# Kernel tuning notes

Measured on AMD Instinct MI355X. Metric: run time of the kernel, lower is better.

## Reference

```python
import jax, jax.numpy as jnp
import numpy as np

N, E, L, HEADS, HID = 50000, 600000, 4, 8, 128
IN_C, OUT_C = 64, 64
D_HEAD = HID // HEADS


def _layer_norm(x, g, b, eps=1e-5):
    m = jnp.mean(x, axis=-1, keepdims=True)
    v = jnp.mean((x - m) ** 2, axis=-1, keepdims=True)
    return (x - m) * jax.lax.rsqrt(v + eps) * g + b


def _transformer_conv(h, src, dst, Wq, bq, Wk, bk, Wv, bv, Ws, bs, Wbeta):
    # PyG TransformerConv with beta=True, concat=True. src=edge_index[0] (j), dst=edge_index[1] (i).
    n, f = h.shape
    q = (h @ Wq.T + bq)[dst].reshape(-1, HEADS, D_HEAD)   # [E,H,D] query at destination
    k = (h @ Wk.T + bk)[src].reshape(-1, HEADS, D_HEAD)   # [E,H,D] key at source
    v = (h @ Wv.T + bv)[src].reshape(-1, HEADS, D_HEAD)   # [E,H,D] value at source
    alpha = jnp.sum(q * k, axis=-1) / float(np.sqrt(D_HEAD))  # [E,H]
    amax = jax.ops.segment_max(alpha, dst, num_segments=n)     # [N,H] segment softmax (stable)
    ex = jnp.exp(alpha - amax[dst])
    denom = jax.ops.segment_sum(ex, dst, num_segments=n)
    a = ex / (denom[dst] + 1e-16)                              # [E,H]
    out = jax.ops.segment_sum((a[:, :, None] * v).reshape(-1, f), dst, num_segments=n)  # [N,F]
    x_r = h @ Ws.T + bs                                        # root/skip transform
    beta = jax.nn.sigmoid(jnp.concatenate([out, x_r, out - x_r], axis=-1) @ Wbeta.T)    # [N,1]
    return beta * x_r + (1.0 - beta) * out


def _forward(x, src, dst, Wi, bi, Wq, bq, Wk, bk, Wv, bv, Ws, bs, Wbeta, ln_g, ln_b, W1, b1, W2, b2, Wo, bo):
    h = jax.nn.gelu(x @ Wi.T + bi, approximate=False)
    for i in range(L):
        res = h
        h = _transformer_conv(h, src, dst, Wq[i], bq[i], Wk[i], bk[i], Wv[i], bv[i], Ws[i], bs[i], Wbeta[i])
        h = _layer_norm(h + res, ln_g[i], ln_b[i])
        res = h
        f = jax.nn.gelu(h @ W1[i].T + b1[i], approximate=False) @ W2[i].T + b2[i]
        h = f + res
    return h @ Wo.T + bo


def setup_inputs() -> dict:
    key = jax.random.key(0)
    ks = jax.random.split(key, 24)
    rn = lambda k, shp, s=0.05: (jax.random.normal(k, shp, jnp.float32) * s)
    x = jax.random.normal(ks[0], (N, IN_C), jnp.float32)
    edge_index = jax.random.randint(ks[1], (2, E), 0, N, dtype=jnp.int64)
    return {
        "x": x,
        "edge_index": edge_index,
        "Wi": rn(ks[2], (HID, IN_C)), "bi": jnp.zeros((HID,), jnp.float32),
        "Wq": rn(ks[3], (L, HID, HID)), "bq": jnp.zeros((L, HID), jnp.float32),
        "Wk": rn(ks[4], (L, HID, HID)), "bk": jnp.zeros((L, HID), jnp.float32),
        "Wv": rn(ks[5], (L, HID, HID)), "bv": jnp.zeros((L, HID), jnp.float32),
        "Ws": rn(ks[6], (L, HID, HID)), "bs": jnp.zeros((L, HID), jnp.float32),
        "Wbeta": rn(ks[7], (L, 1, 3 * HID)),
        "ln_g": jnp.ones((L, HID), jnp.float32), "ln_b": jnp.zeros((L, HID), jnp.float32),
        "W1": rn(ks[8], (L, 4 * HID, HID)), "b1": jnp.zeros((L, 4 * HID), jnp.float32),
        "W2": rn(ks[9], (L, HID, 4 * HID)), "b2": jnp.zeros((L, HID), jnp.float32),
        "Wo": rn(ks[10], (OUT_C, HID)), "bo": jnp.zeros((OUT_C,), jnp.float32),
    }


def reference(x, edge_index, Wi, bi, Wq, bq, Wk, bk, Wv, bv, Ws, bs, Wbeta, ln_g, ln_b, W1, b1, W2, b2, Wo, bo):
    src, dst = edge_index[0], edge_index[1]
    return _forward(x, src, dst, Wi, bi, Wq, bq, Wk, bk, Wv, bv, Ws, bs, Wbeta, ln_g, ln_b, W1, b1, W2, b2, Wo, bo)
```

## Files before the change

### kernel.cpp

```cpp
#include <hip/hip_runtime.h>
#include <cmath>

#define HIDC   128
#define LAYERS 4
#define IN_C   64
#define OUT_C  64

typedef _Float16 h16x8 __attribute__((ext_vector_type(8)));
typedef float    f32x4 __attribute__((ext_vector_type(4)));

__device__ __forceinline__ float gelu_f(float x) {
    return 0.5f * x * (1.0f + erff(x * 0.70710678118654752f));
}

__device__ __forceinline__ void cvt8(const float4& a, const float4& b, h16x8& h) {
    h[0]=(_Float16)a.x; h[1]=(_Float16)a.y; h[2]=(_Float16)a.z; h[3]=(_Float16)a.w;
    h[4]=(_Float16)b.x; h[5]=(_Float16)b.y; h[6]=(_Float16)b.z; h[7]=(_Float16)b.w;
}
__device__ __forceinline__ void load16(const float* p, _Float16* d) {
    float4 v0 = *(const float4*)p,     v1 = *(const float4*)(p + 4);
    float4 v2 = *(const float4*)(p+8), v3 = *(const float4*)(p + 12);
    h16x8 h0, h1; cvt8(v0, v1, h0); cvt8(v2, v3, h1);
    *(h16x8*)d = h0; *(h16x8*)(d + 8) = h1;
}
__device__ __forceinline__ void load16(const _Float16* p, _Float16* d) {
    *(h16x8*)d = *(const h16x8*)p; *(h16x8*)(d + 8) = *(const h16x8*)(p + 8);
}
__device__ __forceinline__ void zero16(_Float16* d) {
    h16x8 z = {};
    *(h16x8*)d = z; *(h16x8*)(d + 8) = z;
}

__global__ void count_deg_k(const int* __restrict__ dst, int* __restrict__ cnt, int E) {
    int i = blockIdx.x * blockDim.x + threadIdx.x;
    if (i < E) atomicAdd(&cnt[dst[i]], 1);
}

__global__ __launch_bounds__(256)
void scan1_k(const int* __restrict__ cnt, int* __restrict__ pref,
             int* __restrict__ bsum, int n) {
    __shared__ int part[256];
    const int b = blockIdx.x, t = threadIdx.x;
    const int i0 = b * 1024 + t * 4;
    int v0 = (i0 + 0 < n) ? cnt[i0 + 0] : 0;
    int v1 = (i0 + 1 < n) ? cnt[i0 + 1] : 0;
    int v2 = (i0 + 2 < n) ? cnt[i0 + 2] : 0;
    int v3 = (i0 + 3 < n) ? cnt[i0 + 3] : 0;
    int s = v0 + v1 + v2 + v3;
    part[t] = s;
    __syncthreads();
    for (int off = 1; off < 256; off <<= 1) {
        int x = (t >= off) ? part[t - off] : 0;
        __syncthreads();
        part[t] += x;
        __syncthreads();
    }
    int excl = part[t] - s;
    if (i0 + 0 < n) pref[i0 + 0] = excl;           excl += v0;
    if (i0 + 1 < n) pref[i0 + 1] = excl;           excl += v1;
    if (i0 + 2 < n) pref[i0 + 2] = excl;           excl += v2;
    if (i0 + 3 < n) pref[i0 + 3] = excl;
    if (t == 255) bsum[b] = part[255];
}

__global__ void scan2_k(const int* __restrict__ bsum, int* __restrict__ boff,
                        int nb, int* __restrict__ rowptr_n) {
    int lane = threadIdx.x;
    int carry = 0;
    for (int base = 0; base < nb; base += 64) {
        int i = base + lane;
        int v = (i < nb) ? bsum[i] : 0;
        int incl = v;
        for (int off = 1; off < 64; off <<= 1) {
            int x = __shfl_up(incl, off);
            if (lane >= off) incl += x;
        }
        if (i < nb) boff[i] = carry + incl - v;
        carry += __shfl(incl, 63);
    }
    if (lane == 0) *rowptr_n = carry;
}

__global__ __launch_bounds__(256)
void scan3_k(int* __restrict__ pref, const int* __restrict__ boff, int n) {
    int i = blockIdx.x * blockDim.x + threadIdx.x;
    if (i < n) pref[i] += boff[i >> 10];
}

__global__ void scatter_k(const int* __restrict__ src, const int* __restrict__ dst,
                          const int* __restrict__ rowptr, int* __restrict__ cnt,
                          int* __restrict__ csrc, int E) {
    int i = blockIdx.x * blockDim.x + threadIdx.x;
    if (i < E) {
        int d = dst[i];
        int pos = rowptr[d] + atomicAdd(&cnt[d], 1);
        csrc[pos] = src[i];
    }
}

template<int ACT, bool RES, bool NGUARD, typename AT, typename CT>
__device__ __forceinline__ void gemm_core(
    const AT* __restrict__ A, const float* __restrict__ Wt,
    const float* __restrict__ bias, const float* __restrict__ resid,
    CT* __restrict__ Ct, int M, int K, int ncs, int colbase, int nclim)
{
    __shared__ __align__(16) _Float16 As[128 * 40];
    __shared__ __align__(16) _Float16 Bs[128 * 40];
    const int tid  = threadIdx.x;
    const int lane = tid & 63;
    const int wave = tid >> 6;
    const int wr = wave >> 1, wc = wave & 1;
    const int row0 = blockIdx.y * 128;

    f32x4 acc[4][4] = {};

    const int srow = tid >> 1;
    const int skc  = (tid & 1) * 16;
    const int fr   = lane & 15;
    const int fk   = (lane >> 4) * 8;

    for (int k0 = 0; k0 < K; k0 += 32) {
        {
            int gr = row0 + srow;
            _Float16* d = As + srow * 40 + skc;
            if (gr < M) load16(A + (size_t)gr * K + k0 + skc, d);
            else        zero16(d);
        }
        {
            int gc = colbase + srow;
            _Float16* d = Bs + srow * 40 + skc;
            if (!NGUARD || gc < nclim) load16(Wt + (size_t)gc * K + k0 + skc, d);
            else                       zero16(d);
        }
        __syncthreads();
        h16x8 af[4], bf[4];
#pragma unroll
        for (int mi = 0; mi < 4; ++mi)
            af[mi] = *(const h16x8*)(As + (wr * 64 + mi * 16 + fr) * 40 + fk);
#pragma unroll
        for (int ni = 0; ni < 4; ++ni)
            bf[ni] = *(const h16x8*)(Bs + (wc * 64 + ni * 16 + fr) * 40 + fk);
#pragma unroll
        for (int mi = 0; mi < 4; ++mi)
#pragma unroll
            for (int ni = 0; ni < 4; ++ni)
                acc[mi][ni] = __builtin_amdgcn_mfma_f32_16x16x32_f16(af[mi], bf[ni], acc[mi][ni], 0, 0, 0);
        __syncthreads();
    }

    const int rbase = row0 + wr * 64 + ((lane >> 4) * 4);
    const int cbase = colbase + wc * 64 + fr;
#pragma unroll
    for (int mi = 0; mi < 4; ++mi) {
#pragma unroll
        for (int j = 0; j < 4; ++j) {
            int r = rbase + mi * 16 + j;
            if (r >= M) continue;
            size_t rb = (size_t)r * ncs;
#pragma unroll
            for (int ni = 0; ni < 4; ++ni) {
                int c = cbase + ni * 16;
                if (NGUARD && c >= nclim) continue;
                float v = acc[mi][ni][j] + bias[c];
                if (ACT == 1) v = gelu_f(v);
                if (RES) v += resid[rb + c];
                Ct[rb + c] = (CT)v;
            }
        }
    }
}

template<int ACT, bool RES, bool NGUARD, typename AT, typename CT>
__global__ __launch_bounds__(256)
void gemm_f16_k(const AT* __restrict__ A, const float* __restrict__ W,
                const float* __restrict__ bias, const float* __restrict__ resid,
                CT* __restrict__ C, int M, int NC, int K) {
    gemm_core<ACT, RES, NGUARD, AT, CT>(A, W, bias, resid, C, M, K, NC, blockIdx.x * 128, NC);
}

__global__ __launch_bounds__(256)
void qkvs_k(const float* __restrict__ A,
            const float* __restrict__ Wq, const float* __restrict__ Wk,
            const float* __restrict__ Wv, const float* __restrict__ Wvs,
            const float* __restrict__ bq, const float* __restrict__ bk,
            const float* __restrict__ bv, const float* __restrict__ bs,
            _Float16* __restrict__ qh, _Float16* __restrict__ kv,
            float* __restrict__ sb, int M) {
    __shared__ __align__(16) _Float16 As[128 * 40];
    __shared__ __align__(16) _Float16 Bs[128 * 40];
    const int proj = blockIdx.x;
    const float* Wt = (proj == 0) ? Wq : (proj == 1) ? Wk : (proj == 2) ? Wv : Wvs;
    const float* bp = (proj == 0) ? bq : (proj == 1) ? bk : (proj == 2) ? bv : bs;

    const int tid  = threadIdx.x;
    const int lane = tid & 63;
    const int wave = tid >> 6;
    const int wr = wave >> 1, wc = wave & 1;
    const int row0 = blockIdx.y * 128;

    f32x4 acc[4][4] = {};

    const int srow = tid >> 1;
    const int skc  = (tid & 1) * 16;
    const int fr   = lane & 15;
    const int fk   = (lane >> 4) * 8;

    for (int k0 = 0; k0 < 128; k0 += 32) {
        {
            int gr = row0 + srow;
            _Float16* d = As + srow * 40 + skc;
            if (gr < M) load16(A + (size_t)gr * 128 + k0 + skc, d);
            else        zero16(d);
        }
        {
            _Float16* d = Bs + srow * 40 + skc;
            load16(Wt + (size_t)srow * 128 + k0 + skc, d);
        }
        __syncthreads();
        h16x8 af[4], bf[4];
#pragma unroll
        for (int mi = 0; mi < 4; ++mi)
            af[mi] = *(const h16x8*)(As + (wr * 64 + mi * 16 + fr) * 40 + fk);
#pragma unroll
        for (int ni = 0; ni < 4; ++ni)
            bf[ni] = *(const h16x8*)(Bs + (wc * 64 + ni * 16 + fr) * 40 + fk);
#pragma unroll
        for (int mi = 0; mi < 4; ++mi)
#pragma unroll
            for (int ni = 0; ni < 4; ++ni)
                acc[mi][ni] = __builtin_amdgcn_mfma_f32_16x16x32_f16(af[mi], bf[ni], acc[mi][ni], 0, 0, 0);
        __syncthreads();
    }

    const int rbase = row0 + wr * 64 + ((lane >> 4) * 4);
    const int cbase = wc * 64 + fr;
#pragma unroll
    for (int mi = 0; mi < 4; ++mi) {
#pragma unroll
        for (int j = 0; j < 4; ++j) {
            int r = rbase + mi * 16 + j;
            if (r >= M) continue;
#pragma unroll
            for (int ni = 0; ni < 4; ++ni) {
                int c = cbase + ni * 16;
                float v = acc[mi][ni][j] + bp[c];
                if (proj == 0)      qh[(size_t)r * 128 + c] = (_Float16)v;
                else if (proj == 1) kv[(size_t)r * 256 + c] = (_Float16)v;
                else if (proj == 2) kv[(size_t)r * 256 + 128 + c] = (_Float16)v;
                else                sb[(size_t)r * 128 + c] = v;
            }
        }
    }
}

__global__ __launch_bounds__(256)
void attn_ln_k(const _Float16* __restrict__ qh, const _Float16* __restrict__ kv,
               const int* __restrict__ rowptr, const int* __restrict__ csrc,
               const float* __restrict__ xr, const float* __restrict__ res,
               const float* __restrict__ Wb, const float* __restrict__ g_,
               const float* __restrict__ b_, float* __restrict__ out, int n) {
    int node = (int)((blockIdx.x * (size_t)blockDim.x + threadIdx.x) >> 6);
    int lane = threadIdx.x & 63;
    if (node >= n) return;
    const int g = lane & 7;
    const int h = lane >> 3;

    const _Float16* qp = qh + (size_t)node * 128 + h * 16;
    h16x8 q0 = *(const h16x8*)(qp);
    h16x8 q1 = *(const h16x8*)(qp + 8);

    float ssum = 0.f;
    float acc[16] = {};
    const int e0 = rowptr[node], e1 = rowptr[node + 1];
    for (int eb = e0; eb < e1; eb += 8) {
        int e = eb + g;
        bool val = (e < e1);
        int s = csrc[val ? e : (e1 - 1)];
        const _Float16* kp = kv + (size_t)s * 256 + h * 16;
        h16x8 k0 = *(const h16x8*)(kp);
        h16x8 k1 = *(const h16x8*)(kp + 8);
        h16x8 v0 = *(const h16x8*)(kp + 128);
        h16x8 v1 = *(const h16x8*)(kp + 136);
        float d = 0.f;
#pragma unroll
        for (int j = 0; j < 8; ++j) d += (float)k0[j] * (float)q0[j];
#pragma unroll
        for (int j = 0; j < 8; ++j) d += (float)k1[j] * (float)q1[j];
        float w = val ? __expf(d * 0.25f) : 0.f;
        ssum += w;
#pragma unroll
        for (int j = 0; j < 8; ++j) acc[j]     += w * (float)v0[j];
#pragma unroll
        for (int j = 0; j < 8; ++j) acc[8 + j] += w * (float)v1[j];
    }
#pragma unroll
    for (int m = 1; m < 8; m <<= 1) {
        ssum += __shfl_xor(ssum, m);
#pragma unroll
        for (int j = 0; j < 16; ++j) acc[j] += __shfl_xor(acc[j], m);
    }
    float inv = 1.f / (ssum + 1e-16f);
    const bool s0b = g & 1, s1b = g & 2, s2b = g & 4;
    float t0 = s0b ? acc[2]  : acc[0],  t1 = s0b ? acc[6]  : acc[4];
    float t2 = s0b ? acc[10] : acc[8],  t3 = s0b ? acc[14] : acc[12];
    float u0 = s1b ? t1 : t0,           u1 = s1b ? t3 : t2;
    float ox = (s2b ? u1 : u0) * inv;
    float p0 = s0b ? acc[3]  : acc[1],  p1 = s0b ? acc[7]  : acc[5];
    float p2 = s0b ? acc[11] : acc[9],  p3 = s0b ? acc[15] : acc[13];
    float w0 = s1b ? p1 : p0,           w1 = s1b ? p3 : p2;
    float oy = (s2b ? w1 : w0) * inv;

    size_t base = (size_t)node * HIDC + lane * 2;
    int c = lane * 2;
    float2 r  = *(const float2*)(xr + base);
    float2 wb0 = *(const float2*)(Wb + c);
    float2 wb1 = *(const float2*)(Wb + HIDC + c);
    float2 wb2 = *(const float2*)(Wb + 2 * HIDC + c);
    float part = ox * wb0.x + oy * wb0.y
               + r.x * wb1.x + r.y * wb1.y
               + (ox - r.x) * wb2.x + (oy - r.y) * wb2.y;
#pragma unroll
    for (int mk = 1; mk < 64; mk <<= 1) part += __shfl_xor(part, mk);
    float beta = 1.f / (1.f + __expf(-part));
    float2 rs = *(const float2*)(res + base);
    float tx = beta * r.x + (1.f - beta) * ox + rs.x;
    float ty = beta * r.y + (1.f - beta) * oy + rs.y;
    float sum = tx + ty;
#pragma unroll
    for (int mk = 1; mk < 64; mk <<= 1) sum += __shfl_xor(sum, mk);
    float mean = sum * (1.f / 128.f);
    float dx = tx - mean, dy = ty - mean;
    float vs = dx * dx + dy * dy;
#pragma unroll
    for (int mk = 1; mk < 64; mk <<= 1) vs += __shfl_xor(vs, mk);
    float rstd = 1.f / sqrtf(vs * (1.f / 128.f) + 1e-5f);
    float2 gg = *(const float2*)(g_ + c);
    float2 bb = *(const float2*)(b_ + c);
    float2 oo = make_float2(dx * rstd * gg.x + bb.x, dy * rstd * gg.y + bb.y);
    *(float2*)(out + base) = oo;
}

extern "C" void kernel_launch(void* const* d_in, const int* in_sizes, int n_in,
                              void* d_out, int out_size, void* d_ws, size_t ws_size,
                              hipStream_t stream) {
    const float* x    = (const float*)d_in[0];
    const int*   ei   = (const int*)d_in[1];
    const float* Wi   = (const float*)d_in[2];
    const float* bi   = (const float*)d_in[3];
    const float* Wq   = (const float*)d_in[4];
    const float* bq   = (const float*)d_in[5];
    const float* Wk   = (const float*)d_in[6];
    const float* bk   = (const float*)d_in[7];
    const float* Wv   = (const float*)d_in[8];
    const float* bv   = (const float*)d_in[9];
    const float* Ws_  = (const float*)d_in[10];
    const float* bs   = (const float*)d_in[11];
    const float* Wbeta= (const float*)d_in[12];
    const float* ln_g = (const float*)d_in[13];
    const float* ln_b = (const float*)d_in[14];
    const float* W1   = (const float*)d_in[15];
    const float* b1   = (const float*)d_in[16];
    const float* W2   = (const float*)d_in[17];
    const float* b2   = (const float*)d_in[18];
    const float* Wo   = (const float*)d_in[19];
    const float* bo   = (const float*)d_in[20];
    float* outp = (float*)d_out;

    const int Nn = in_sizes[0] / IN_C;
    const int Ee = in_sizes[1] / 2;
    const int* srcI = ei;
    const int* dstI = ei + Ee;

    float* ws = (float*)d_ws;
    size_t n128 = (size_t)Nn * HIDC;
    float*     h   = ws;
    float*     h2  = h  + n128;
    _Float16*  qh  = (_Float16*)(h2 + n128);
    _Float16*  kv  = qh + (size_t)Nn * 128;
    float*     sb  = (float*)(kv + (size_t)Nn * 256);
    _Float16*  ffn = qh;
    int* rowptr = (int*)(sb + n128);
    int* cnt    = rowptr + (Nn + 1);
    int* csrc   = cnt + Nn;
    int* bsum   = csrc + Ee;
    int* boff   = bsum + 1024;

    const int nb = (Nn + 1023) / 1024;

    hipMemsetAsync(cnt, 0, Nn * sizeof(int), stream);
    count_deg_k<<<(Ee + 255) / 256, 256, 0, stream>>>(dstI, cnt, Ee);
    scan1_k<<<nb, 256, 0, stream>>>(cnt, rowptr, bsum, Nn);
    scan2_k<<<1, 64, 0, stream>>>(bsum, boff, nb, rowptr + Nn);
    scan3_k<<<(Nn + 255) / 256, 256, 0, stream>>>(rowptr, boff, Nn);
    hipMemsetAsync(cnt, 0, Nn * sizeof(int), stream);
    scatter_k<<<(Ee + 255) / 256, 256, 0, stream>>>(srcI, dstI, rowptr, cnt, csrc, Ee);

    const int mblk = (Nn + 127) / 128;
    dim3 blk(256);

    gemm_f16_k<1, false, false, float, float><<<dim3(1, mblk), blk, 0, stream>>>(x, Wi, bi, nullptr, h, Nn, HIDC, IN_C);

    int nwaveblk = (Nn + 3) / 4;

    for (int l = 0; l < LAYERS; ++l) {
        const float* Wq_l = Wq + (size_t)l * HIDC * HIDC;
        const float* Wk_l = Wk + (size_t)l * HIDC * HIDC;
        const float* Wv_l = Wv + (size_t)l * HIDC * HIDC;
        const float* Ws_l = Ws_ + (size_t)l * HIDC * HIDC;
        const float* bq_l = bq + (size_t)l * HIDC;
        const float* bk_l = bk + (size_t)l * HIDC;
        const float* bv_l = bv + (size_t)l * HIDC;
        const float* bs_l = bs + (size_t)l * HIDC;
        const float* Wb_l = Wbeta + (size_t)l * 3 * HIDC;
        const float* g_l  = ln_g + (size_t)l * HIDC;
        const float* b_l  = ln_b + (size_t)l * HIDC;
        const float* W1_l = W1 + (size_t)l * 4 * HIDC * HIDC;
        const float* b1_l = b1 + (size_t)l * 4 * HIDC;
        const float* W2_l = W2 + (size_t)l * HIDC * 4 * HIDC;
        const float* b2_l = b2 + (size_t)l * HIDC;

        qkvs_k<<<dim3(4, mblk), blk, 0, stream>>>(h, Wq_l, Wk_l, Wv_l, Ws_l,
                                                  bq_l, bk_l, bv_l, bs_l,
                                                  qh, kv, sb, Nn);

        attn_ln_k<<<nwaveblk, blk, 0, stream>>>(qh, kv, rowptr, csrc,
                                                sb, h, Wb_l, g_l, b_l, h2, Nn);

        gemm_f16_k<1, false, false, float, _Float16><<<dim3(4, mblk), blk, 0, stream>>>(h2, W1_l, b1_l, nullptr, ffn, Nn, 4 * HIDC, HIDC);
        gemm_f16_k<0, true, false, _Float16, float><<<dim3(1, mblk), blk, 0, stream>>>(ffn, W2_l, b2_l, h2, h, Nn, HIDC, 4 * HIDC);
    }

    gemm_f16_k<0, false, true, float, float><<<dim3(1, mblk), blk, 0, stream>>>(h, Wo, bo, nullptr, outp, Nn, OUT_C, HIDC);
}
```

Before: 1.076 ms.

## Double-buffer GEMM shared-memory tiles and store skip projection in fp16

Both GEMM paths (generic and fused QKVS) now prefetch the next K-slice into registers while MFMAs run on the current shared-memory buffer. Alternating between two LDS buffers removes one barrier per iteration. The skip projection x_r is also written and read as fp16 instead of fp32, which halves that tensor's traffic between qkvs_k and attn_ln_k. The costs are doubled LDS use per block, which may lower occupancy, more registers held for the prefetch, and reduced precision on x_r.

```diff
diff --git a/kernel.cpp b/kernel.cpp
--- a/kernel.cpp
+++ b/kernel.cpp
@@ -7,6 +7,7 @@
 #define OUT_C  64
 
 typedef _Float16 h16x8 __attribute__((ext_vector_type(8)));
+typedef _Float16 h16x2 __attribute__((ext_vector_type(2)));
 typedef float    f32x4 __attribute__((ext_vector_type(4)));
 
 __device__ __forceinline__ float gelu_f(float x) {
@@ -17,19 +18,30 @@
     h[0]=(_Float16)a.x; h[1]=(_Float16)a.y; h[2]=(_Float16)a.z; h[3]=(_Float16)a.w;
     h[4]=(_Float16)b.x; h[5]=(_Float16)b.y; h[6]=(_Float16)b.z; h[7]=(_Float16)b.w;
 }
-__device__ __forceinline__ void load16(const float* p, _Float16* d) {
-    float4 v0 = *(const float4*)p,     v1 = *(const float4*)(p + 4);
-    float4 v2 = *(const float4*)(p+8), v3 = *(const float4*)(p + 12);
-    h16x8 h0, h1; cvt8(v0, v1, h0); cvt8(v2, v3, h1);
-    *(h16x8*)d = h0; *(h16x8*)(d + 8) = h1;
-}
-__device__ __forceinline__ void load16(const _Float16* p, _Float16* d) {
-    *(h16x8*)d = *(const h16x8*)p; *(h16x8*)(d + 8) = *(const h16x8*)(p + 8);
-}
-__device__ __forceinline__ void zero16(_Float16* d) {
-    h16x8 z = {};
-    *(h16x8*)d = z; *(h16x8*)(d + 8) = z;
-}
+
+template<typename T> struct RegT;
+template<> struct RegT<float> {
+    float4 v[4];
+    __device__ __forceinline__ void fetch(const float* p) {
+        v[0]=*(const float4*)p;     v[1]=*(const float4*)(p+4);
+        v[2]=*(const float4*)(p+8); v[3]=*(const float4*)(p+12);
+    }
+    __device__ __forceinline__ void store(_Float16* d) const {
+        h16x8 h0,h1; cvt8(v[0],v[1],h0); cvt8(v[2],v[3],h1);
+        *(h16x8*)d=h0; *(h16x8*)(d+8)=h1;
+    }
+    __device__ __forceinline__ void zero() { v[0]=v[1]=v[2]=v[3]=make_float4(0.f,0.f,0.f,0.f); }
+};
+template<> struct RegT<_Float16> {
+    h16x8 v[2];
+    __device__ __forceinline__ void fetch(const _Float16* p) {
+        v[0]=*(const h16x8*)p; v[1]=*(const h16x8*)(p+8);
+    }
+    __device__ __forceinline__ void store(_Float16* d) const {
+        *(h16x8*)d=v[0]; *(h16x8*)(d+8)=v[1];
+    }
+    __device__ __forceinline__ void zero() { h16x8 z={}; v[0]=z; v[1]=z; }
+};
 
 __global__ void count_deg_k(const int* __restrict__ dst, int* __restrict__ cnt, int E) {
     int i = blockIdx.x * blockDim.x + threadIdx.x;
@@ -104,8 +116,8 @@
     const float* __restrict__ bias, const float* __restrict__ resid,
     CT* __restrict__ Ct, int M, int K, int ncs, int colbase, int nclim)
 {
-    __shared__ __align__(16) _Float16 As[128 * 40];
-    __shared__ __align__(16) _Float16 Bs[128 * 40];
+    __shared__ __align__(16) _Float16 As[2][128 * 40];
+    __shared__ __align__(16) _Float16 Bs[2][128 * 40];
     const int tid  = threadIdx.x;
     const int lane = tid & 63;
     const int wave = tid >> 6;
@@ -119,33 +131,44 @@
     const int fr   = lane & 15;
     const int fk   = (lane >> 4) * 8;
 
-    for (int k0 = 0; k0 < K; k0 += 32) {
-        {
-            int gr = row0 + srow;
-            _Float16* d = As + srow * 40 + skc;
-            if (gr < M) load16(A + (size_t)gr * K + k0 + skc, d);
-            else        zero16(d);
-        }
-        {
-            int gc = colbase + srow;
-            _Float16* d = Bs + srow * 40 + skc;
-            if (!NGUARD || gc < nclim) load16(Wt + (size_t)gc * K + k0 + skc, d);
-            else                       zero16(d);
-        }
+    const int gr = row0 + srow;
+    const bool ga = (gr < M);
+    const int gc = colbase + srow;
+    const bool gb = (!NGUARD || gc < nclim);
+    const AT*    pa = A  + (size_t)gr * K + skc;
+    const float* pb = Wt + (size_t)gc * K + skc;
+
+    RegT<AT>    ra;
+    RegT<float> rb;
+    if (ga) ra.fetch(pa); else ra.zero();
+    if (gb) rb.fetch(pb); else rb.zero();
+    ra.store(As[0] + srow * 40 + skc);
+    rb.store(Bs[0] + srow * 40 + skc);
+
+    const int nk = K >> 5;
+    for (int kk = 0; kk < nk; ++kk) {
+        const int cur = kk & 1;
         __syncthreads();
+        if (kk + 1 < nk) {
+            if (ga) ra.fetch(pa + (kk + 1) * 32);
+            if (gb) rb.fetch(pb + (kk + 1) * 32);
+        }
         h16x8 af[4], bf[4];
 #pragma unroll
         for (int mi = 0; mi < 4; ++mi)
-            af[mi] = *(const h16x8*)(As + (wr * 64 + mi * 16 + fr) * 40 + fk);
+            af[mi] = *(const h16x8*)(As[cur] + (wr * 64 + mi * 16 + fr) * 40 + fk);
 #pragma unroll
         for (int ni = 0; ni < 4; ++ni)
-            bf[ni] = *(const h16x8*)(Bs + (wc * 64 + ni * 16 + fr) * 40 + fk);
+            bf[ni] = *(const h16x8*)(Bs[cur] + (wc * 64 + ni * 16 + fr) * 40 + fk);
 #pragma unroll
         for (int mi = 0; mi < 4; ++mi)
 #pragma unroll
             for (int ni = 0; ni < 4; ++ni)
                 acc[mi][ni] = __builtin_amdgcn_mfma_f32_16x16x32_f16(af[mi], bf[ni], acc[mi][ni], 0, 0, 0);
-        __syncthreads();
+        if (kk + 1 < nk) {
+            ra.store(As[cur ^ 1] + srow * 40 + skc);
+            rb.store(Bs[cur ^ 1] + srow * 40 + skc);
+        }
     }
 
     const int rbase = row0 + wr * 64 + ((lane >> 4) * 4);
@@ -156,15 +179,15 @@
         for (int j = 0; j < 4; ++j) {
             int r = rbase + mi * 16 + j;
             if (r >= M) continue;
-            size_t rb = (size_t)r * ncs;
+            size_t rb2 = (size_t)r * ncs;
 #pragma unroll
             for (int ni = 0; ni < 4; ++ni) {
                 int c = cbase + ni * 16;
                 if (NGUARD && c >= nclim) continue;
                 float v = acc[mi][ni][j] + bias[c];
                 if (ACT == 1) v = gelu_f(v);
-                if (RES) v += resid[rb + c];
-                Ct[rb + c] = (CT)v;
+                if (RES) v += resid[rb2 + c];
+                Ct[rb2 + c] = (CT)v;
             }
         }
     }
@@ -185,9 +208,9 @@
             const float* __restrict__ bq, const float* __restrict__ bk,
             const float* __restrict__ bv, const float* __restrict__ bs,
             _Float16* __restrict__ qh, _Float16* __restrict__ kv,
-            float* __restrict__ sb, int M) {
-    __shared__ __align__(16) _Float16 As[128 * 40];
-    __shared__ __align__(16) _Float16 Bs[128 * 40];
+            _Float16* __restrict__ sbh, int M) {
+    __shared__ __align__(16) _Float16 As[2][128 * 40];
+    __shared__ __align__(16) _Float16 Bs[2][128 * 40];
     const int proj = blockIdx.x;
     const float* Wt = (proj == 0) ? Wq : (proj == 1) ? Wk : (proj == 2) ? Wv : Wvs;
     const float* bp = (proj == 0) ? bq : (proj == 1) ? bk : (proj == 2) ? bv : bs;
@@ -205,31 +228,40 @@
     const int fr   = lane & 15;
     const int fk   = (lane >> 4) * 8;
 
-    for (int k0 = 0; k0 < 128; k0 += 32) {
-        {
-            int gr = row0 + srow;
-            _Float16* d = As + srow * 40 + skc;
-            if (gr < M) load16(A + (size_t)gr * 128 + k0 + skc, d);
-            else        zero16(d);
-        }
-        {
-            _Float16* d = Bs + srow * 40 + skc;
-            load16(Wt + (size_t)srow * 128 + k0 + skc, d);
-        }
+    const int gr = row0 + srow;
+    const bool ga = (gr < M);
+    const float* pa = A  + (size_t)gr * 128 + skc;
+    const float* pb = Wt + (size_t)srow * 128 + skc;
+
+    RegT<float> ra, rb;
+    if (ga) ra.fetch(pa); else ra.zero();
+    rb.fetch(pb);
+    ra.store(As[0] + srow * 40 + skc);
+    rb.store(Bs[0] + srow * 40 + skc);
+
+    for (int kk = 0; kk < 4; ++kk) {
+        const int cur = kk & 1;
         __syncthreads();
+        if (kk + 1 < 4) {
+            if (ga) ra.fetch(pa + (kk + 1) * 32);
+            rb.fetch(pb + (kk + 1) * 32);
+        }
         h16x8 af[4], bf[4];
 #pragma unroll
         for (int mi = 0; mi < 4; ++mi)
-            af[mi] = *(const h16x8*)(As + (wr * 64 + mi * 16 + fr) * 40 + fk);
+            af[mi] = *(const h16x8*)(As[cur] + (wr * 64 + mi * 16 + fr) * 40 + fk);
 #pragma unroll
         for (int ni = 0; ni < 4; ++ni)
-            bf[ni] = *(const h16x8*)(Bs + (wc * 64 + ni * 16 + fr) * 40 + fk);
+            bf[ni] = *(const h16x8*)(Bs[cur] + (wc * 64 + ni * 16 + fr) * 40 + fk);
 #pragma unroll
         for (int mi = 0; mi < 4; ++mi)
 #pragma unroll
             for (int ni = 0; ni < 4; ++ni)
                 acc[mi][ni] = __builtin_amdgcn_mfma_f32_16x16x32_f16(af[mi], bf[ni], acc[mi][ni], 0, 0, 0);
-        __syncthreads();
+        if (kk + 1 < 4) {
+            ra.store(As[cur ^ 1] + srow * 40 + skc);
+            rb.store(Bs[cur ^ 1] + srow * 40 + skc);
+        }
     }
 
     const int rbase = row0 + wr * 64 + ((lane >> 4) * 4);
@@ -247,7 +279,7 @@
                 if (proj == 0)      qh[(size_t)r * 128 + c] = (_Float16)v;
                 else if (proj == 1) kv[(size_t)r * 256 + c] = (_Float16)v;
                 else if (proj == 2) kv[(size_t)r * 256 + 128 + c] = (_Float16)v;
-                else                sb[(size_t)r * 128 + c] = v;
+                else                sbh[(size_t)r * 128 + c] = (_Float16)v;
             }
         }
     }
@@ -256,7 +288,7 @@
 __global__ __launch_bounds__(256)
 void attn_ln_k(const _Float16* __restrict__ qh, const _Float16* __restrict__ kv,
                const int* __restrict__ rowptr, const int* __restrict__ csrc,
-               const float* __restrict__ xr, const float* __restrict__ res,
+               const _Float16* __restrict__ xr, const float* __restrict__ res,
                const float* __restrict__ Wb, const float* __restrict__ g_,
                const float* __restrict__ b_, float* __restrict__ out, int n) {
     int node = (int)((blockIdx.x * (size_t)blockDim.x + threadIdx.x) >> 6);
@@ -312,19 +344,20 @@
 
     size_t base = (size_t)node * HIDC + lane * 2;
     int c = lane * 2;
-    float2 r  = *(const float2*)(xr + base);
+    h16x2 xv = *(const h16x2*)(xr + base);
+    float rx = (float)xv[0], ry = (float)xv[1];
     float2 wb0 = *(const float2*)(Wb + c);
     float2 wb1 = *(const float2*)(Wb + HIDC + c);
     float2 wb2 = *(const float2*)(Wb + 2 * HIDC + c);
     float part = ox * wb0.x + oy * wb0.y
-               + r.x * wb1.x + r.y * wb1.y
-               + (ox - r.x) * wb2.x + (oy - r.y) * wb2.y;
+               + rx * wb1.x + ry * wb1.y
+               + (ox - rx) * wb2.x + (oy - ry) * wb2.y;
 #pragma unroll
     for (int mk = 1; mk < 64; mk <<= 1) part += __shfl_xor(part, mk);
     float beta = 1.f / (1.f + __expf(-part));
     float2 rs = *(const float2*)(res + base);
-    float tx = beta * r.x + (1.f - beta) * ox + rs.x;
-    float ty = beta * r.y + (1.f - beta) * oy + rs.y;
+    float tx = beta * rx + (1.f - beta) * ox + rs.x;
+    float ty = beta * ry + (1.f - beta) * oy + rs.y;
     float sum = tx + ty;
 #pragma unroll
     for (int mk = 1; mk < 64; mk <<= 1) sum += __shfl_xor(sum, mk);
@@ -377,9 +410,9 @@
     float*     h2  = h  + n128;
     _Float16*  qh  = (_Float16*)(h2 + n128);
     _Float16*  kv  = qh + (size_t)Nn * 128;
-    float*     sb  = (float*)(kv + (size_t)Nn * 256);
+    _Float16*  sbh = kv + (size_t)Nn * 256;
     _Float16*  ffn = qh;
-    int* rowptr = (int*)(sb + n128);
+    int* rowptr = (int*)(h2 + n128 + 2 * n128);
     int* cnt    = rowptr + (Nn + 1);
     int* csrc   = cnt + Nn;
     int* bsum   = csrc + Ee;
@@ -421,10 +454,10 @@
 
         qkvs_k<<<dim3(4, mblk), blk, 0, stream>>>(h, Wq_l, Wk_l, Wv_l, Ws_l,
                                                   bq_l, bk_l, bv_l, bs_l,
-                                                  qh, kv, sb, Nn);
+                                                  qh, kv, sbh, Nn);
 
         attn_ln_k<<<nwaveblk, blk, 0, stream>>>(qh, kv, rowptr, csrc,
-                                                sb, h, Wb_l, g_l, b_l, h2, Nn);
+                                                sbh, h, Wb_l, g_l, b_l, h2, Nn);
 
         gemm_f16_k<1, false, false, float, _Float16><<<dim3(4, mblk), blk, 0, stream>>>(h2, W1_l, b1_l, nullptr, ffn, Nn, 4 * HIDC, HIDC);
         gemm_f16_k<0, true, false, _Float16, float><<<dim3(1, mblk), blk, 0, stream>>>(ffn, W2_l, b2_l, h2, h, Nn, HIDC, 4 * HIDC);
```

New measurement: 1.082 ms. No clear change (+0.6%).

## Store activations in fp16 and replace LDS-tiled GEMMs with direct-load MFMA kernels

Applied to the files above, without the earlier changes.

Converts inputs and all weight matrices to fp16 up front, keeps every intermediate activation (h, h2, skip projection) in fp16, and replaces the shared-memory tiled GEMM with a kernel where each wave loads A and W fragments directly from global memory into MFMA operands. This removes LDS staging, the barriers and the per-tile fp32-to-fp16 conversion, and halves activation traffic. In exchange weights are re-read from global/L2 per wave with no LDS reuse, nine conversion kernels run on every call, and residual/LayerNorm paths lose precision by storing in fp16.

```diff
diff --git a/kernel.cpp b/kernel.cpp
--- a/kernel.cpp
+++ b/kernel.cpp
@@ -7,6 +7,7 @@
 #define OUT_C  64
 
 typedef _Float16 h16x8 __attribute__((ext_vector_type(8)));
+typedef _Float16 h16x2 __attribute__((ext_vector_type(2)));
 typedef float    f32x4 __attribute__((ext_vector_type(4)));
 
 __device__ __forceinline__ float gelu_f(float x) {
@@ -17,18 +18,17 @@
     h[0]=(_Float16)a.x; h[1]=(_Float16)a.y; h[2]=(_Float16)a.z; h[3]=(_Float16)a.w;
     h[4]=(_Float16)b.x; h[5]=(_Float16)b.y; h[6]=(_Float16)b.z; h[7]=(_Float16)b.w;
 }
-__device__ __forceinline__ void load16(const float* p, _Float16* d) {
-    float4 v0 = *(const float4*)p,     v1 = *(const float4*)(p + 4);
-    float4 v2 = *(const float4*)(p+8), v3 = *(const float4*)(p + 12);
-    h16x8 h0, h1; cvt8(v0, v1, h0); cvt8(v2, v3, h1);
-    *(h16x8*)d = h0; *(h16x8*)(d + 8) = h1;
-}
-__device__ __forceinline__ void load16(const _Float16* p, _Float16* d) {
-    *(h16x8*)d = *(const h16x8*)p; *(h16x8*)(d + 8) = *(const h16x8*)(p + 8);
-}
-__device__ __forceinline__ void zero16(_Float16* d) {
-    h16x8 z = {};
-    *(h16x8*)d = z; *(h16x8*)(d + 8) = z;
+
+__global__ __launch_bounds__(256)
+void cvtf16_k(const float* __restrict__ s, _Float16* __restrict__ d, int n) {
+    int i = (blockIdx.x * blockDim.x + threadIdx.x) * 8;
+    if (i + 8 <= n) {
+        float4 a = *(const float4*)(s + i), b = *(const float4*)(s + i + 4);
+        h16x8 h; cvt8(a, b, h);
+        *(h16x8*)(d + i) = h;
+    } else {
+        for (int j = i; j < n; ++j) d[j] = (_Float16)s[j];
+    }
 }
 
 __global__ void count_deg_k(const int* __restrict__ dst, int* __restrict__ cnt, int E) {
@@ -98,167 +98,85 @@
     }
 }
 
-template<int ACT, bool RES, bool NGUARD, typename AT, typename CT>
-__device__ __forceinline__ void gemm_core(
-    const AT* __restrict__ A, const float* __restrict__ Wt,
-    const float* __restrict__ bias, const float* __restrict__ resid,
-    CT* __restrict__ Ct, int M, int K, int ncs, int colbase, int nclim)
+template<int ACT, bool RES, int CTN, int KT, typename CT>
+__device__ __forceinline__ void gdirect(
+    const _Float16* __restrict__ A, const _Float16* __restrict__ W,
+    const float* __restrict__ bias, const _Float16* __restrict__ resid,
+    CT* __restrict__ Cp, int M, int ncs, int wave, int lane, int rowblk)
 {
-    __shared__ __align__(16) _Float16 As[128 * 40];
-    __shared__ __align__(16) _Float16 Bs[128 * 40];
-    const int tid  = threadIdx.x;
-    const int lane = tid & 63;
-    const int wave = tid >> 6;
-    const int wr = wave >> 1, wc = wave & 1;
-    const int row0 = blockIdx.y * 128;
-
-    f32x4 acc[4][4] = {};
-
-    const int srow = tid >> 1;
-    const int skc  = (tid & 1) * 16;
-    const int fr   = lane & 15;
-    const int fk   = (lane >> 4) * 8;
-
-    for (int k0 = 0; k0 < K; k0 += 32) {
-        {
-            int gr = row0 + srow;
-            _Float16* d = As + srow * 40 + skc;
-            if (gr < M) load16(A + (size_t)gr * K + k0 + skc, d);
-            else        zero16(d);
+    const int r0  = rowblk * 64 + wave * 16;
+    const int l15 = lane & 15;
+    const int kof = (lane >> 4) * 8;
+    int arow = r0 + l15; if (arow >= M) arow = M - 1;
+    const _Float16* ap = A + (size_t)arow * KT + kof;
+    const _Float16* wp = W + (size_t)l15 * KT + kof;
+
+    f32x4 acc[CTN] = {};
+#pragma unroll
+    for (int kk = 0; kk < KT / 32; ++kk) {
+        h16x8 af = *(const h16x8*)(ap + kk * 32);
+#pragma unroll
+        for (int ct = 0; ct < CTN; ++ct) {
+            h16x8 bf = *(const h16x8*)(wp + (size_t)ct * 16 * KT + kk * 32);
+            acc[ct] = __builtin_amdgcn_mfma_f32_16x16x32_f16(af, bf, acc[ct], 0, 0, 0);
         }
-        {
-            int gc = colbase + srow;
-            _Float16* d = Bs + srow * 40 + skc;
-            if (!NGUARD || gc < nclim) load16(Wt + (size_t)gc * K + k0 + skc, d);
-            else                       zero16(d);
+    }
+
+    const int rb = r0 + (lane >> 4) * 4;
+#pragma unroll
+    for (int j = 0; j < 4; ++j) {
+        int r = rb + j;
+        if (r >= M) continue;
+        size_t ro = (size_t)r * ncs;
+#pragma unroll
+        for (int ct = 0; ct < CTN; ++ct) {
+            int c = ct * 16 + l15;
+            float v = acc[ct][j] + bias[c];
+            if (ACT) v = gelu_f(v);
+            if (RES) v += (float)resid[ro + c];
+            Cp[ro + c] = (CT)v;
         }
-        __syncthreads();
-        h16x8 af[4], bf[4];
-#pragma unroll
-        for (int mi = 0; mi < 4; ++mi)
-            af[mi] = *(const h16x8*)(As + (wr * 64 + mi * 16 + fr) * 40 + fk);
-#pragma unroll
-        for (int ni = 0; ni < 4; ++ni)
-            bf[ni] = *(const h16x8*)(Bs + (wc * 64 + ni * 16 + fr) * 40 + fk);
-#pragma unroll
-        for (int mi = 0; mi < 4; ++mi)
-#pragma unroll
-            for (int ni = 0; ni < 4; ++ni)
-                acc[mi][ni] = __builtin_amdgcn_mfma_f32_16x16x32_f16(af[mi], bf[ni], acc[mi][ni], 0, 0, 0);
-        __syncthreads();
-    }
-
-    const int rbase = row0 + wr * 64 + ((lane >> 4) * 4);
-    const int cbase = colbase + wc * 64 + fr;
-#pragma unroll
-    for (int mi = 0; mi < 4; ++mi) {
-#pragma unroll
-        for (int j = 0; j < 4; ++j) {
-            int r = rbase + mi * 16 + j;
-            if (r >= M) continue;
-            size_t rb = (size_t)r * ncs;
-#pragma unroll
-            for (int ni = 0; ni < 4; ++ni) {
-                int c = cbase + ni * 16;
-                if (NGUARD && c >= nclim) continue;
-                float v = acc[mi][ni][j] + bias[c];
-                if (ACT == 1) v = gelu_f(v);
-                if (RES) v += resid[rb + c];
-                Ct[rb + c] = (CT)v;
-            }
-        }
-    }
-}
-
-template<int ACT, bool RES, bool NGUARD, typename AT, typename CT>
-__global__ __launch_bounds__(256)
-void gemm_f16_k(const AT* __restrict__ A, const float* __restrict__ W,
-                const float* __restrict__ bias, const float* __restrict__ resid,
-                CT* __restrict__ C, int M, int NC, int K) {
-    gemm_core<ACT, RES, NGUARD, AT, CT>(A, W, bias, resid, C, M, K, NC, blockIdx.x * 128, NC);
-}
-
-__global__ __launch_bounds__(256)
-void qkvs_k(const float* __restrict__ A,
-            const float* __restrict__ Wq, const float* __restrict__ Wk,
-            const float* __restrict__ Wv, const float* __restrict__ Wvs,
-            const float* __restrict__ bq, const float* __restrict__ bk,
-            const float* __restrict__ bv, const float* __restrict__ bs,
-            _Float16* __restrict__ qh, _Float16* __restrict__ kv,
-            float* __restrict__ sb, int M) {
-    __shared__ __align__(16) _Float16 As[128 * 40];
-    __shared__ __align__(16) _Float16 Bs[128 * 40];
+    }
+}
+
+template<int ACT, bool RES, int CTN, int KT, typename CT>
+__global__ __launch_bounds__(256)
+void gemm_dir_k(const _Float16* __restrict__ A, const _Float16* __restrict__ W,
+                const float* __restrict__ bias, const _Float16* __restrict__ resid,
+                CT* __restrict__ C, int M, int ncs) {
+    const int lane = threadIdx.x & 63, wave = threadIdx.x >> 6;
+    const size_t cb = (size_t)blockIdx.x * (CTN * 16);
+    gdirect<ACT, RES, CTN, KT, CT>(A, W + cb * KT, bias + cb,
+                                   resid ? resid + cb : resid, C + cb,
+                                   M, ncs, wave, lane, blockIdx.y);
+}
+
+__global__ __launch_bounds__(256)
+void qkvs_dir_k(const _Float16* __restrict__ A,
+                const _Float16* __restrict__ Wq, const _Float16* __restrict__ Wk,
+                const _Float16* __restrict__ Wv, const _Float16* __restrict__ Ws,
+                const float* __restrict__ bq, const float* __restrict__ bk,
+                const float* __restrict__ bv, const float* __restrict__ bs,
+                _Float16* __restrict__ qh, _Float16* __restrict__ kv,
+                _Float16* __restrict__ sbh, int M) {
+    const int lane = threadIdx.x & 63, wave = threadIdx.x >> 6;
     const int proj = blockIdx.x;
-    const float* Wt = (proj == 0) ? Wq : (proj == 1) ? Wk : (proj == 2) ? Wv : Wvs;
-    const float* bp = (proj == 0) ? bq : (proj == 1) ? bk : (proj == 2) ? bv : bs;
-
-    const int tid  = threadIdx.x;
-    const int lane = tid & 63;
-    const int wave = tid >> 6;
-    const int wr = wave >> 1, wc = wave & 1;
-    const int row0 = blockIdx.y * 128;
-
-    f32x4 acc[4][4] = {};
-
-    const int srow = tid >> 1;
-    const int skc  = (tid & 1) * 16;
-    const int fr   = lane & 15;
-    const int fk   = (lane >> 4) * 8;
-
-    for (int k0 = 0; k0 < 128; k0 += 32) {
-        {
-            int gr = row0 + srow;
-            _Float16* d = As + srow * 40 + skc;
-            if (gr < M) load16(A + (size_t)gr * 128 + k0 + skc, d);
-            else        zero16(d);
-        }
-        {
-            _Float16* d = Bs + srow * 40 + skc;
-            load16(Wt + (size_t)srow * 128 + k0 + skc, d);
-        }
-        __syncthreads();
-        h16x8 af[4], bf[4];
-#pragma unroll
-        for (int mi = 0; mi < 4; ++mi)
-            af[mi] = *(const h16x8*)(As + (wr * 64 + mi * 16 + fr) * 40 + fk);
-#pragma unroll
-        for (int ni = 0; ni < 4; ++ni)
-            bf[ni] = *(const h16x8*)(Bs + (wc * 64 + ni * 16 + fr) * 40 + fk);
-#pragma unroll
-        for (int mi = 0; mi < 4; ++mi)
-#pragma unroll
-            for (int ni = 0; ni < 4; ++ni)
-                acc[mi][ni] = __builtin_amdgcn_mfma_f32_16x16x32_f16(af[mi], bf[ni], acc[mi][ni], 0, 0, 0);
-        __syncthreads();
-    }
-
-    const int rbase = row0 + wr * 64 + ((lane >> 4) * 4);
-    const int cbase = wc * 64 + fr;
-#pragma unroll
-    for (int mi = 0; mi < 4; ++mi) {
-#pragma unroll
-        for (int j = 0; j < 4; ++j) {
-            int r = rbase + mi * 16 + j;
-            if (r >= M) continue;
-#pragma unroll
-            for (int ni = 0; ni < 4; ++ni) {
-                int c = cbase + ni * 16;
-                float v = acc[mi][ni][j] + bp[c];
-                if (proj == 0)      qh[(size_t)r * 128 + c] = (_Float16)v;
-                else if (proj == 1) kv[(size_t)r * 256 + c] = (_Float16)v;
-                else if (proj == 2) kv[(size_t)r * 256 + 128 + c] = (_Float16)v;
-                else                sb[(size_t)r * 128 + c] = v;
-            }
-        }
-    }
+    const _Float16* W = (proj == 0) ? Wq : (proj == 1) ? Wk : (proj == 2) ? Wv : Ws;
+    const float*    b = (proj == 0) ? bq : (proj == 1) ? bk : (proj == 2) ? bv : bs;
+    _Float16* out; int ncs;
+    if      (proj == 0) { out = qh;       ncs = 128; }
+    else if (proj == 1) { out = kv;       ncs = 256; }
+    else if (proj == 2) { out = kv + 128; ncs = 256; }
+    else                { out = sbh;      ncs = 128; }
+    gdirect<0, false, 8, 128, _Float16>(A, W, b, nullptr, out, M, ncs, wave, lane, blockIdx.y);
 }
 
 __global__ __launch_bounds__(256)
 void attn_ln_k(const _Float16* __restrict__ qh, const _Float16* __restrict__ kv,
                const int* __restrict__ rowptr, const int* __restrict__ csrc,
-               const float* __restrict__ xr, const float* __restrict__ res,
+               const _Float16* __restrict__ xr, const _Float16* __restrict__ res,
                const float* __restrict__ Wb, const float* __restrict__ g_,
-               const float* __restrict__ b_, float* __restrict__ out, int n) {
+               const float* __restrict__ b_, _Float16* __restrict__ out, int n) {
     int node = (int)((blockIdx.x * (size_t)blockDim.x + threadIdx.x) >> 6);
     int lane = threadIdx.x & 63;
     if (node >= n) return;
@@ -312,19 +230,20 @@
 
     size_t base = (size_t)node * HIDC + lane * 2;
     int c = lane * 2;
-    float2 r  = *(const float2*)(xr + base);
+    h16x2 xv = *(const h16x2*)(xr + base);
+    float rx = (float)xv[0], ry = (float)xv[1];
     float2 wb0 = *(const float2*)(Wb + c);
     float2 wb1 = *(const float2*)(Wb + HIDC + c);
     float2 wb2 = *(const float2*)(Wb + 2 * HIDC + c);
     float part = ox * wb0.x + oy * wb0.y
-               + r.x * wb1.x + r.y * wb1.y
-               + (ox - r.x) * wb2.x + (oy - r.y) * wb2.y;
+               + rx * wb1.x + ry * wb1.y
+               + (ox - rx) * wb2.x + (oy - ry) * wb2.y;
 #pragma unroll
     for (int mk = 1; mk < 64; mk <<= 1) part += __shfl_xor(part, mk);
     float beta = 1.f / (1.f + __expf(-part));
-    float2 rs = *(const float2*)(res + base);
-    float tx = beta * r.x + (1.f - beta) * ox + rs.x;
-    float ty = beta * r.y + (1.f - beta) * oy + rs.y;
+    h16x2 rv = *(const h16x2*)(res + base);
+    float tx = beta * rx + (1.f - beta) * ox + (float)rv[0];
+    float ty = beta * ry + (1.f - beta) * oy + (float)rv[1];
     float sum = tx + ty;
 #pragma unroll
     for (int mk = 1; mk < 64; mk <<= 1) sum += __shfl_xor(sum, mk);
@@ -336,8 +255,10 @@
     float rstd = 1.f / sqrtf(vs * (1.f / 128.f) + 1e-5f);
     float2 gg = *(const float2*)(g_ + c);
     float2 bb = *(const float2*)(b_ + c);
-    float2 oo = make_float2(dx * rstd * gg.x + bb.x, dy * rstd * gg.y + bb.y);
-    *(float2*)(out + base) = oo;
+    h16x2 oo;
+    oo[0] = (_Float16)(dx * rstd * gg.x + bb.x);
+    oo[1] = (_Float16)(dy * rstd * gg.y + bb.y);
+    *(h16x2*)(out + base) = oo;
 }
 
 extern "C" void kernel_launch(void* const* d_in, const int* in_sizes, int n_in,
@@ -371,22 +292,43 @@
     const int* srcI = ei;
     const int* dstI = ei + Ee;
 
-    float* ws = (float*)d_ws;
-    size_t n128 = (size_t)Nn * HIDC;
-    float*     h   = ws;
-    float*     h2  = h  + n128;
-    _Float16*  qh  = (_Float16*)(h2 + n128);
-    _Float16*  kv  = qh + (size_t)Nn * 128;
-    float*     sb  = (float*)(kv + (size_t)Nn * 256);
-    _Float16*  ffn = qh;
-    int* rowptr = (int*)(sb + n128);
+    _Float16* f16 = (_Float16*)d_ws;
+    size_t Nf = (size_t)Nn;
+    _Float16* h    = f16;
+    _Float16* h2   = h    + Nf * 128;
+    _Float16* qh   = h2   + Nf * 128;
+    _Float16* kv   = qh   + Nf * 128;
+    _Float16* sbh  = kv   + Nf * 256;
+    _Float16* ffn  = qh;
+    _Float16* xh   = sbh  + Nf * 128;
+    _Float16* Wih  = xh   + Nf * 64;
+    _Float16* Wqh  = Wih  + 128 * 64;
+    _Float16* Wkh  = Wqh  + LAYERS * 128 * 128;
+    _Float16* Wvh  = Wkh  + LAYERS * 128 * 128;
+    _Float16* Wsh  = Wvh  + LAYERS * 128 * 128;
+    _Float16* W1h  = Wsh  + LAYERS * 128 * 128;
+    _Float16* W2h  = W1h  + LAYERS * 512 * 128;
+    _Float16* Woh  = W2h  + LAYERS * 128 * 512;
+    int* rowptr = (int*)(Woh + 64 * 128);
     int* cnt    = rowptr + (Nn + 1);
     int* csrc   = cnt + Nn;
     int* bsum   = csrc + Ee;
     int* boff   = bsum + 1024;
 
+    dim3 blk(256);
+    auto cvtgrid = [](int n) { return dim3((n / 8 + 255) / 256); };
+
+    cvtf16_k<<<cvtgrid(Nn * IN_C), blk, 0, stream>>>(x, xh, Nn * IN_C);
+    cvtf16_k<<<cvtgrid(128 * 64), blk, 0, stream>>>(Wi, Wih, 128 * 64);
+    cvtf16_k<<<cvtgrid(LAYERS * 128 * 128), blk, 0, stream>>>(Wq, Wqh, LAYERS * 128 * 128);
+    cvtf16_k<<<cvtgrid(LAYERS * 128 * 128), blk, 0, stream>>>(Wk, Wkh, LAYERS * 128 * 128);
+    cvtf16_k<<<cvtgrid(LAYERS * 128 * 128), blk, 0, stream>>>(Wv, Wvh, LAYERS * 128 * 128);
+    cvtf16_k<<<cvtgrid(LAYERS * 128 * 128), blk, 0, stream>>>(Ws_, Wsh, LAYERS * 128 * 128);
+    cvtf16_k<<<cvtgrid(LAYERS * 512 * 128), blk, 0, stream>>>(W1, W1h, LAYERS * 512 * 128);
+    cvtf16_k<<<cvtgrid(LAYERS * 128 * 512), blk, 0, stream>>>(W2, W2h, LAYERS * 128 * 512);
+    cvtf16_k<<<cvtgrid(64 * 128), blk, 0, stream>>>(Wo, Woh, 64 * 128);
+
     const int nb = (Nn + 1023) / 1024;
-
     hipMemsetAsync(cnt, 0, Nn * sizeof(int), stream);
     count_deg_k<<<(Ee + 255) / 256, 256, 0, stream>>>(dstI, cnt, Ee);
     scan1_k<<<nb, 256, 0, stream>>>(cnt, rowptr, bsum, Nn);
@@ -395,18 +337,16 @@
     hipMemsetAsync(cnt, 0, Nn * sizeof(int), stream);
     scatter_k<<<(Ee + 255) / 256, 256, 0, stream>>>(srcI, dstI, rowptr, cnt, csrc, Ee);
 
-    const int mblk = (Nn + 127) / 128;
-    dim3 blk(256);
-
-    gemm_f16_k<1, false, false, float, float><<<dim3(1, mblk), blk, 0, stream>>>(x, Wi, bi, nullptr, h, Nn, HIDC, IN_C);
-
+    const int rblk = (Nn + 63) / 64;
     int nwaveblk = (Nn + 3) / 4;
 
+    gemm_dir_k<1, false, 8, 64, _Float16><<<dim3(1, rblk), blk, 0, stream>>>(xh, Wih, bi, nullptr, h, Nn, HIDC);
+
     for (int l = 0; l < LAYERS; ++l) {
-        const float* Wq_l = Wq + (size_t)l * HIDC * HIDC;
-        const float* Wk_l = Wk + (size_t)l * HIDC * HIDC;
-        const float* Wv_l = Wv + (size_t)l * HIDC * HIDC;
-        const float* Ws_l = Ws_ + (size_t)l * HIDC * HIDC;
+        const _Float16* Wq_l = Wqh + (size_t)l * 128 * 128;
+        const _Float16* Wk_l = Wkh + (size_t)l * 128 * 128;
+        const _Float16* Wv_l = Wvh + (size_t)l * 128 * 128;
+        const _Float16* Ws_l = Wsh + (size_t)l * 128 * 128;
         const float* bq_l = bq + (size_t)l * HIDC;
         const float* bk_l = bk + (size_t)l * HIDC;
         const float* bv_l = bv + (size_t)l * HIDC;
@@ -414,21 +354,21 @@
         const float* Wb_l = Wbeta + (size_t)l * 3 * HIDC;
         const float* g_l  = ln_g + (size_t)l * HIDC;
         const float* b_l  = ln_b + (size_t)l * HIDC;
-        const float* W1_l = W1 + (size_t)l * 4 * HIDC * HIDC;
+        const _Float16* W1_l = W1h + (size_t)l * 512 * 128;
+        const _Float16* W2_l = W2h + (size_t)l * 128 * 512;
         const float* b1_l = b1 + (size_t)l * 4 * HIDC;
-        const float* W2_l = W2 + (size_t)l * HIDC * 4 * HIDC;
         const float* b2_l = b2 + (size_t)l * HIDC;
 
-        qkvs_k<<<dim3(4, mblk), blk, 0, stream>>>(h, Wq_l, Wk_l, Wv_l, Ws_l,
-                                                  bq_l, bk_l, bv_l, bs_l,
-                                                  qh, kv, sb, Nn);
+        qkvs_dir_k<<<dim3(4, rblk), blk, 0, stream>>>(h, Wq_l, Wk_l, Wv_l, Ws_l,
+                                                      bq_l, bk_l, bv_l, bs_l,
+                                                      qh, kv, sbh, Nn);
 
         attn_ln_k<<<nwaveblk, blk, 0, stream>>>(qh, kv, rowptr, csrc,
-                                                sb, h, Wb_l, g_l, b_l, h2, Nn);
-
-        gemm_f16_k<1, false, false, float, _Float16><<<dim3(4, mblk), blk, 0, stream>>>(h2, W1_l, b1_l, nullptr, ffn, Nn, 4 * HIDC, HIDC);
-        gemm_f16_k<0, true, false, _Float16, float><<<dim3(1, mblk), blk, 0, stream>>>(ffn, W2_l, b2_l, h2, h, Nn, HIDC, 4 * HIDC);
-    }
-
-    gemm_f16_k<0, false, true, float, float><<<dim3(1, mblk), blk, 0, stream>>>(h, Wo, bo, nullptr, outp, Nn, OUT_C, HIDC);
-}
+                                                sbh, h, Wb_l, g_l, b_l, h2, Nn);
+
+        gemm_dir_k<1, false, 8, 128, _Float16><<<dim3(4, rblk), blk, 0, stream>>>(h2, W1_l, b1_l, nullptr, ffn, Nn, 4 * HIDC);
+        gemm_dir_k<0, true, 8, 512, _Float16><<<dim3(1, rblk), blk, 0, stream>>>(ffn, W2_l, b2_l, h2, h, Nn, HIDC);
+    }
+
+    gemm_dir_k<0, false, 4, 128, float><<<dim3(1, rblk), blk, 0, stream>>>(h, Woh, bo, nullptr, outp, Nn, OUT_C);
+}
```

Result: slower. 1.294 ms (+20.3%).
